# Performance work log

Hardware: AMD Instinct MI355X
Metric: run time of the kernel (lower is better)

Reference implementation:

```python
import jax, jax.numpy as jnp
import numpy as np

B, T, IN, CELL, OUT = 512, 32, 512, 128, 128


def setup_inputs() -> dict:
    key = jax.random.key(0)
    ks = jax.random.split(key, 6)
    d = IN + CELL
    w = lambda k, shape, fan: jax.random.normal(k, shape, jnp.float32) / np.sqrt(fan).astype(np.float32)
    return {
        "x": jax.random.normal(ks[0], (B, T, IN), jnp.float32),
        "Wf": w(ks[1], (d, CELL), d), "bf": jnp.zeros((CELL,), jnp.float32),
        "Wi1": w(ks[2], (d, CELL), d), "bi1": jnp.zeros((CELL,), jnp.float32),
        "Wi2": w(ks[3], (d, CELL), d), "bi2": jnp.zeros((CELL,), jnp.float32),
        "Wo": w(ks[4], (d, CELL), d), "bo": jnp.zeros((CELL,), jnp.float32),
        "Wc": w(ks[5], (CELL, OUT), CELL), "bc": jnp.zeros((OUT,), jnp.float32),
    }


def reference(x, Wf, bf, Wi1, bi1, Wi2, bi2, Wo, bo, Wc, bc):
    # Faithful to MyLSTM.forward: loop runs x.shape[1] times; each iteration
    # concatenates the FULL [B,T,CELL] cell_state with the FULL [B,T,IN] x
    # (x is never sliced per step). Only the last iteration's output matters,
    # but we carry it through the scan to match the loop structure exactly.
    Tn = x.shape[1]
    c0 = jnp.zeros(x.shape[:2] + (Wf.shape[1],), x.dtype)
    out0 = jnp.zeros(x.shape[:2] + (Wc.shape[1],), x.dtype)

    def step(carry, _):
        c, _prev_out = carry
        inp = jnp.concatenate([c, x], axis=-1)  # [B,T,CELL+IN]
        f = jax.nn.sigmoid(inp @ Wf + bf)
        c = c * f + jax.nn.sigmoid(inp @ Wi1 + bi1) * jnp.tanh(inp @ Wi2 + bi2)
        o = jax.nn.sigmoid(inp @ Wo + bo) * jnp.tanh(c)
        out = jax.nn.softmax(o @ Wc + bc, axis=2)  # out_features != 1 branch
        return (c, out), None

    (c, out), _ = jax.lax.scan(step, (c0, out0), None, length=Tn)
    return out, c
```

## Files before the change

### kernel.cpp

```cpp
#include <hip/hip_runtime.h>
#include <stdint.h>

#define ROWS  16384
#define CELL  128
#define INF   512
#define RPB   16
#define NSTEP 32

typedef _Float16 f16x8 __attribute__((ext_vector_type(8)));
typedef _Float16 f16x4 __attribute__((ext_vector_type(4)));
typedef float    f32x4 __attribute__((ext_vector_type(4)));

#define MFMA16(a, b, c) __builtin_amdgcn_mfma_f32_16x16x32_f16((a), (b), (c), 0, 0, 0)

#define AOFF  0
#define XOFF  65536
#define WCOFF 327680
#define WSTOT 344064

#define LOG2E  1.44269504f
#define LOG2E2 2.88539008f

__device__ __forceinline__ unsigned short f2h_bits(float f) {
  _Float16 h = (_Float16)f;
  return *(unsigned short*)&h;
}
__device__ __forceinline__ float sig2(float z) {
  return __builtin_amdgcn_rcpf(1.f + __builtin_amdgcn_exp2f(-z));
}
__device__ __forceinline__ float tanh2(float z) {
  return 1.f - 2.f * __builtin_amdgcn_rcpf(__builtin_amdgcn_exp2f(z) + 1.f);
}

__global__ __launch_bounds__(256) void prep_kernel(
    const float* __restrict__ Wf, const float* __restrict__ Wi1,
    const float* __restrict__ Wi2, const float* __restrict__ Wo,
    const float* __restrict__ Wc, unsigned short* __restrict__ ws) {
  int id = blockIdx.x * blockDim.x + threadIdx.x;
  if (id >= WSTOT) return;
  const float* Wg[4] = {Wf, Wi1, Wi2, Wo};
  const float scl[4] = {LOG2E, LOG2E, LOG2E2, LOG2E};
  float v;
  int k, n, base;
  if (id < XOFF) {
    int g = id >> 14, r = id & 16383;
    k = r >> 7; n = r & 127;
    v = Wg[g][k * CELL + n] * scl[g];
    base = g * 16384;
  } else if (id < WCOFF) {
    int t = id - XOFF;
    int g = t >> 16, r = t & 65535;
    k = r >> 7; n = r & 127;
    v = Wg[g][(CELL + k) * CELL + n] * scl[g];
    base = XOFF + g * 65536;
  } else {
    int r = id - WCOFF;
    k = r >> 7; n = r & 127;
    v = Wc[k * CELL + n];
    base = WCOFF;
  }
  int ks = k >> 5, kk = k & 31;
  int lane = ((kk >> 3) << 4) | (n & 15);
  int j = kk & 7, nb = n >> 4;
  ws[base + ((ks * 8 + nb) * 64 + lane) * 8 + j] = f2h_bits(v);
}

__global__ __launch_bounds__(512, 4) void lstm_kernel(
    const float* __restrict__ x,
    const float* __restrict__ bf_, const float* __restrict__ bi1,
    const float* __restrict__ bi2, const float* __restrict__ bo,
    const float* __restrict__ bc,
    const unsigned short* __restrict__ ws, float* __restrict__ out) {

  __shared__ _Float16 cF[2][16][136];
  __shared__ union {
    _Float16 xs[16][520];
    struct {
      float    s[16][132];
      _Float16 o[16][136];
    } ep;
  } uS;

  const int tid  = threadIdx.x;
  const int lane = tid & 63;
  const int w    = tid >> 6;
  const int n16  = lane & 15;
  const int g4   = lane >> 4;
  const int col0 = w * 16 + g4 * 4;
  const int r0   = blockIdx.x * RPB;

  const _Float16* Aw  = (const _Float16*)ws + AOFF;
  const _Float16* Xw  = (const _Float16*)ws + XOFF;
  const _Float16* Wcw = (const _Float16*)ws + WCOFF;

  {
    const float* xb = x + (size_t)r0 * INF;
#pragma unroll
    for (int i = 0; i < 4; ++i) {
      int flat = tid + i * 512;
      int row = flat >> 7, c4 = flat & 127;
      const float4 v = ((const float4*)(xb + (size_t)row * INF))[c4];
      f16x4 h = {(_Float16)v.x, (_Float16)v.y, (_Float16)v.z, (_Float16)v.w};
      *(f16x4*)&uS.xs[row][c4 * 4] = h;
    }
  }
  __syncthreads();

  f32x4 u[4];
#pragma unroll
  for (int g = 0; g < 4; ++g)
#pragma unroll
    for (int i = 0; i < 4; ++i) u[g][i] = 0.f;

#pragma unroll 4
  for (int ks = 0; ks < 16; ++ks) {
    f16x8 a = *(const f16x8*)&uS.xs[n16][ks * 32 + g4 * 8];
#pragma unroll
    for (int g = 0; g < 4; ++g) {
      f16x8 b = *(const f16x8*)(Xw + g * 65536 + ((ks * 8 + w) * 64 + lane) * 8);
      u[g] = MFMA16(b, a, u[g]);
    }
  }
  {
    f32x4 b0 = *(const f32x4*)&bf_[col0];
    f32x4 b1 = *(const f32x4*)&bi1[col0];
    f32x4 b2 = *(const f32x4*)&bi2[col0];
    f32x4 b3 = *(const f32x4*)&bo[col0];
#pragma unroll
    for (int i = 0; i < 4; ++i) {
      u[0][i] = fmaf(b0[i], LOG2E,  u[0][i]);
      u[1][i] = fmaf(b1[i], LOG2E,  u[1][i]);
      u[2][i] = fmaf(b2[i], LOG2E2, u[2][i]);
      u[3][i] = fmaf(b3[i], LOG2E,  u[3][i]);
    }
  }

  f16x8 wr[3][4];
#pragma unroll
  for (int g = 0; g < 3; ++g)
#pragma unroll
    for (int ks = 0; ks < 4; ++ks)
      wr[g][ks] = *(const f16x8*)(Aw + g * 16384 + ((ks * 8 + w) * 64 + lane) * 8);

  f32x4 cr;
  {
    f16x4 hv;
#pragma unroll
    for (int i = 0; i < 4; ++i) {
      float c0 = sig2(u[1][i]) * tanh2(u[2][i]);
      cr[i] = c0;
      hv[i] = (_Float16)c0;
    }
    *(f16x4*)&cF[0][n16][col0] = hv;
  }
  __syncthreads();

#pragma unroll 1
  for (int t = 1; t < NSTEP - 1; ++t) {
    const int rb = (t + 1) & 1, wb = t & 1;
    f16x8 a[4];
#pragma unroll
    for (int ks = 0; ks < 4; ++ks)
      a[ks] = *(const f16x8*)&cF[rb][n16][ks * 32 + g4 * 8];
    f32x4 zf = u[0], zi1 = u[1], zi2 = u[2];
#pragma unroll
    for (int ks = 0; ks < 4; ++ks) {
      zf  = MFMA16(wr[0][ks], a[ks], zf);
      zi1 = MFMA16(wr[1][ks], a[ks], zi1);
      zi2 = MFMA16(wr[2][ks], a[ks], zi2);
    }
    f16x4 hv;
#pragma unroll
    for (int i = 0; i < 4; ++i) {
      float fg = sig2(zf[i]);
      float ig = sig2(zi1[i]);
      float gg = tanh2(zi2[i]);
      float cn = fmaf(cr[i], fg, ig * gg);
      cr[i] = cn;
      hv[i] = (_Float16)cn;
    }
    *(f16x4*)&cF[wb][n16][col0] = hv;
    __syncthreads();
  }

  {
    f16x8 a[4];
#pragma unroll
    for (int ks = 0; ks < 4; ++ks)
      a[ks] = *(const f16x8*)&cF[0][n16][ks * 32 + g4 * 8];
    f32x4 zf = u[0], zi1 = u[1], zi2 = u[2], zo = u[3];
#pragma unroll
    for (int ks = 0; ks < 4; ++ks) {
      f16x8 bo_frag = *(const f16x8*)(Aw + 3 * 16384 + ((ks * 8 + w) * 64 + lane) * 8);
      zf  = MFMA16(wr[0][ks], a[ks], zf);
      zi1 = MFMA16(wr[1][ks], a[ks], zi1);
      zi2 = MFMA16(wr[2][ks], a[ks], zi2);
      zo  = MFMA16(bo_frag,  a[ks], zo);
    }
    f16x4 hv;
#pragma unroll
    for (int i = 0; i < 4; ++i) {
      float fg = sig2(zf[i]);
      float ig = sig2(zi1[i]);
      float gg = tanh2(zi2[i]);
      float cn = fmaf(cr[i], fg, ig * gg);
      cr[i] = cn;
      float ov = sig2(zo[i]) * tanh2(cn * LOG2E2);
      hv[i] = (_Float16)ov;
    }
    __syncthreads();
    *(f16x4*)&uS.ep.o[n16][col0] = hv;
    __syncthreads();
  }

  {
    f32x4 sacc;
#pragma unroll
    for (int i = 0; i < 4; ++i) sacc[i] = 0.f;
#pragma unroll
    for (int ks = 0; ks < 4; ++ks) {
      f16x8 a = *(const f16x8*)&uS.ep.o[n16][ks * 32 + g4 * 8];
      f16x8 b = *(const f16x8*)(Wcw + ((ks * 8 + w) * 64 + lane) * 8);
      sacc = MFMA16(b, a, sacc);
    }
    f32x4 bcv = *(const f32x4*)&bc[col0];
#pragma unroll
    for (int i = 0; i < 4; ++i) sacc[i] += bcv[i];
    *(f32x4*)&uS.ep.s[n16][col0] = sacc;
    __syncthreads();

#pragma unroll
    for (int rr = 0; rr < 2; ++rr) {
      int r = w * 2 + rr;
      float v0 = uS.ep.s[r][lane];
      float v1 = uS.ep.s[r][lane + 64];
      float m = fmaxf(v0, v1);
#pragma unroll
      for (int off = 32; off; off >>= 1) m = fmaxf(m, __shfl_xor(m, off, 64));
      float e0 = __expf(v0 - m), e1 = __expf(v1 - m);
      float sm = e0 + e1;
#pragma unroll
      for (int off = 32; off; off >>= 1) sm += __shfl_xor(sm, off, 64);
      float inv = __builtin_amdgcn_rcpf(sm);
      size_t base = (size_t)(r0 + r) * 128;
      out[base + lane]      = e0 * inv;
      out[base + lane + 64] = e1 * inv;
    }

    *(f32x4*)&out[(size_t)ROWS * 128 + (size_t)(r0 + n16) * 128 + col0] = cr;
  }
}

extern "C" void kernel_launch(void* const* d_in, const int* in_sizes, int n_in,
                              void* d_out, int out_size, void* d_ws, size_t ws_size,
                              hipStream_t stream) {
  const float* x   = (const float*)d_in[0];
  const float* Wf  = (const float*)d_in[1];
  const float* bf_ = (const float*)d_in[2];
  const float* Wi1 = (const float*)d_in[3];
  const float* bi1 = (const float*)d_in[4];
  const float* Wi2 = (const float*)d_in[5];
  const float* bi2 = (const float*)d_in[6];
  const float* Wo  = (const float*)d_in[7];
  const float* bo  = (const float*)d_in[8];
  const float* Wc  = (const float*)d_in[9];
  const float* bc  = (const float*)d_in[10];
  unsigned short* ws = (unsigned short*)d_ws;
  float* out = (float*)d_out;

  hipLaunchKernelGGL(prep_kernel, dim3((WSTOT + 255) / 256), dim3(256), 0, stream,
                     Wf, Wi1, Wi2, Wo, Wc, ws);
  hipLaunchKernelGGL(lstm_kernel, dim3(ROWS / RPB), dim3(512), 0, stream,
                     x, bf_, bi1, bi2, bo, bc, ws, out);
}
```

Measured before the change: 168.5 us.

## Split x staging around input GEMM, drop softmax max pass, raise MFMA priority

The x tile load is split in two halves so the second half's fp16 conversion and LDS store happen after the first half of the input-projection MFMAs, overlapping global load latency with compute. The softmax drops the max-reduction by folding log2e into Wc and applying exp2 directly to the logits, relying on the output being a bounded tanh·sigmoid value times small weights. The recurrent MFMA chains are written out explicitly, and s_setprio is raised around them. The final-step Wo fragments are now loaded all at once before the MFMAs. The softmax without max subtraction risks overflow for inputs where logits are large.

```diff
diff --git a/kernel.cpp b/kernel.cpp
--- a/kernel.cpp
+++ b/kernel.cpp
@@ -56,7 +56,7 @@
   } else {
     int r = id - WCOFF;
     k = r >> 7; n = r & 127;
-    v = Wc[k * CELL + n];
+    v = Wc[k * CELL + n] * LOG2E;
     base = WCOFF;
   }
   int ks = k >> 5, kk = k & 31;
@@ -76,7 +76,7 @@
   __shared__ union {
     _Float16 xs[16][520];
     struct {
-      float    s[16][132];
+      float    e[16][132];
       _Float16 o[16][136];
     } ep;
   } uS;
@@ -93,16 +93,21 @@
   const _Float16* Xw  = (const _Float16*)ws + XOFF;
   const _Float16* Wcw = (const _Float16*)ws + WCOFF;
 
-  {
-    const float* xb = x + (size_t)r0 * INF;
-#pragma unroll
-    for (int i = 0; i < 4; ++i) {
-      int flat = tid + i * 512;
-      int row = flat >> 7, c4 = flat & 127;
-      const float4 v = ((const float4*)(xb + (size_t)row * INF))[c4];
-      f16x4 h = {(_Float16)v.x, (_Float16)v.y, (_Float16)v.z, (_Float16)v.w};
-      *(f16x4*)&uS.xs[row][c4 * 4] = h;
-    }
+  const float* xb = x + (size_t)r0 * INF;
+  float4 v0a, v0b, v1a, v1b;
+  {
+    int fa = tid, fb = tid + 512;
+    int ra = fa >> 6, ca = fa & 63;
+    int rb_ = fb >> 6, cb = fb & 63;
+    const float4* pa = (const float4*)(xb + (size_t)ra * INF);
+    const float4* pb = (const float4*)(xb + (size_t)rb_ * INF);
+    v0a = pa[ca];       v0b = pb[cb];
+    v1a = pa[ca + 64];  v1b = pb[cb + 64];
+    f16x4 h;
+    h = (f16x4){(_Float16)v0a.x, (_Float16)v0a.y, (_Float16)v0a.z, (_Float16)v0a.w};
+    *(f16x4*)&uS.xs[ra][ca * 4] = h;
+    h = (f16x4){(_Float16)v0b.x, (_Float16)v0b.y, (_Float16)v0b.z, (_Float16)v0b.w};
+    *(f16x4*)&uS.xs[rb_][cb * 4] = h;
   }
   __syncthreads();
 
@@ -113,7 +118,29 @@
     for (int i = 0; i < 4; ++i) u[g][i] = 0.f;
 
 #pragma unroll 4
-  for (int ks = 0; ks < 16; ++ks) {
+  for (int ks = 0; ks < 8; ++ks) {
+    f16x8 a = *(const f16x8*)&uS.xs[n16][ks * 32 + g4 * 8];
+#pragma unroll
+    for (int g = 0; g < 4; ++g) {
+      f16x8 b = *(const f16x8*)(Xw + g * 65536 + ((ks * 8 + w) * 64 + lane) * 8);
+      u[g] = MFMA16(b, a, u[g]);
+    }
+  }
+
+  {
+    int fa = tid, fb = tid + 512;
+    int ra = fa >> 6, ca = fa & 63;
+    int rb_ = fb >> 6, cb = fb & 63;
+    f16x4 h;
+    h = (f16x4){(_Float16)v1a.x, (_Float16)v1a.y, (_Float16)v1a.z, (_Float16)v1a.w};
+    *(f16x4*)&uS.xs[ra][256 + ca * 4] = h;
+    h = (f16x4){(_Float16)v1b.x, (_Float16)v1b.y, (_Float16)v1b.z, (_Float16)v1b.w};
+    *(f16x4*)&uS.xs[rb_][256 + cb * 4] = h;
+  }
+  __syncthreads();
+
+#pragma unroll 4
+  for (int ks = 8; ks < 16; ++ks) {
     f16x8 a = *(const f16x8*)&uS.xs[n16][ks * 32 + g4 * 8];
 #pragma unroll
     for (int g = 0; g < 4; ++g) {
@@ -157,18 +184,25 @@
 
 #pragma unroll 1
   for (int t = 1; t < NSTEP - 1; ++t) {
-    const int rb = (t + 1) & 1, wb = t & 1;
-    f16x8 a[4];
-#pragma unroll
-    for (int ks = 0; ks < 4; ++ks)
-      a[ks] = *(const f16x8*)&cF[rb][n16][ks * 32 + g4 * 8];
-    f32x4 zf = u[0], zi1 = u[1], zi2 = u[2];
-#pragma unroll
-    for (int ks = 0; ks < 4; ++ks) {
-      zf  = MFMA16(wr[0][ks], a[ks], zf);
-      zi1 = MFMA16(wr[1][ks], a[ks], zi1);
-      zi2 = MFMA16(wr[2][ks], a[ks], zi2);
-    }
+    const _Float16* rd = &cF[(t + 1) & 1][n16][0];
+    f16x8 a0 = *(const f16x8*)(rd + g4 * 8);
+    f16x8 a1 = *(const f16x8*)(rd + 32 + g4 * 8);
+    f16x8 a2 = *(const f16x8*)(rd + 64 + g4 * 8);
+    f16x8 a3 = *(const f16x8*)(rd + 96 + g4 * 8);
+    __builtin_amdgcn_s_setprio(1);
+    f32x4 zf  = MFMA16(wr[0][0], a0, u[0]);
+    f32x4 zi1 = MFMA16(wr[1][0], a0, u[1]);
+    f32x4 zi2 = MFMA16(wr[2][0], a0, u[2]);
+    zf  = MFMA16(wr[0][1], a1, zf);
+    zi1 = MFMA16(wr[1][1], a1, zi1);
+    zi2 = MFMA16(wr[2][1], a1, zi2);
+    zf  = MFMA16(wr[0][2], a2, zf);
+    zi1 = MFMA16(wr[1][2], a2, zi1);
+    zi2 = MFMA16(wr[2][2], a2, zi2);
+    zf  = MFMA16(wr[0][3], a3, zf);
+    zi1 = MFMA16(wr[1][3], a3, zi1);
+    zi2 = MFMA16(wr[2][3], a3, zi2);
+    __builtin_amdgcn_s_setprio(0);
     f16x4 hv;
 #pragma unroll
     for (int i = 0; i < 4; ++i) {
@@ -179,24 +213,38 @@
       cr[i] = cn;
       hv[i] = (_Float16)cn;
     }
-    *(f16x4*)&cF[wb][n16][col0] = hv;
+    *(f16x4*)&cF[t & 1][n16][col0] = hv;
     __syncthreads();
   }
 
   {
-    f16x8 a[4];
-#pragma unroll
-    for (int ks = 0; ks < 4; ++ks)
-      a[ks] = *(const f16x8*)&cF[0][n16][ks * 32 + g4 * 8];
-    f32x4 zf = u[0], zi1 = u[1], zi2 = u[2], zo = u[3];
-#pragma unroll
-    for (int ks = 0; ks < 4; ++ks) {
-      f16x8 bo_frag = *(const f16x8*)(Aw + 3 * 16384 + ((ks * 8 + w) * 64 + lane) * 8);
-      zf  = MFMA16(wr[0][ks], a[ks], zf);
-      zi1 = MFMA16(wr[1][ks], a[ks], zi1);
-      zi2 = MFMA16(wr[2][ks], a[ks], zi2);
-      zo  = MFMA16(bo_frag,  a[ks], zo);
-    }
+    const _Float16* rd = &cF[0][n16][0];
+    f16x8 a0 = *(const f16x8*)(rd + g4 * 8);
+    f16x8 a1 = *(const f16x8*)(rd + 32 + g4 * 8);
+    f16x8 a2 = *(const f16x8*)(rd + 64 + g4 * 8);
+    f16x8 a3 = *(const f16x8*)(rd + 96 + g4 * 8);
+    f16x8 bo0 = *(const f16x8*)(Aw + 3 * 16384 + ((0 * 8 + w) * 64 + lane) * 8);
+    f16x8 bo1 = *(const f16x8*)(Aw + 3 * 16384 + ((1 * 8 + w) * 64 + lane) * 8);
+    f16x8 bo2 = *(const f16x8*)(Aw + 3 * 16384 + ((2 * 8 + w) * 64 + lane) * 8);
+    f16x8 bo3 = *(const f16x8*)(Aw + 3 * 16384 + ((3 * 8 + w) * 64 + lane) * 8);
+    __builtin_amdgcn_s_setprio(1);
+    f32x4 zf  = MFMA16(wr[0][0], a0, u[0]);
+    f32x4 zi1 = MFMA16(wr[1][0], a0, u[1]);
+    f32x4 zi2 = MFMA16(wr[2][0], a0, u[2]);
+    f32x4 zo  = MFMA16(bo0,      a0, u[3]);
+    zf  = MFMA16(wr[0][1], a1, zf);
+    zi1 = MFMA16(wr[1][1], a1, zi1);
+    zi2 = MFMA16(wr[2][1], a1, zi2);
+    zo  = MFMA16(bo1,      a1, zo);
+    zf  = MFMA16(wr[0][2], a2, zf);
+    zi1 = MFMA16(wr[1][2], a2, zi1);
+    zi2 = MFMA16(wr[2][2], a2, zi2);
+    zo  = MFMA16(bo2,      a2, zo);
+    zf  = MFMA16(wr[0][3], a3, zf);
+    zi1 = MFMA16(wr[1][3], a3, zi1);
+    zi2 = MFMA16(wr[2][3], a3, zi2);
+    zo  = MFMA16(bo3,      a3, zo);
+    __builtin_amdgcn_s_setprio(0);
     f16x4 hv;
 #pragma unroll
     for (int i = 0; i < 4; ++i) {
@@ -224,20 +272,18 @@
       sacc = MFMA16(b, a, sacc);
     }
     f32x4 bcv = *(const f32x4*)&bc[col0];
-#pragma unroll
-    for (int i = 0; i < 4; ++i) sacc[i] += bcv[i];
-    *(f32x4*)&uS.ep.s[n16][col0] = sacc;
+    f32x4 ev;
+#pragma unroll
+    for (int i = 0; i < 4; ++i)
+      ev[i] = __builtin_amdgcn_exp2f(fmaf(bcv[i], LOG2E, sacc[i]));
+    *(f32x4*)&uS.ep.e[n16][col0] = ev;
     __syncthreads();
 
 #pragma unroll
     for (int rr = 0; rr < 2; ++rr) {
       int r = w * 2 + rr;
-      float v0 = uS.ep.s[r][lane];
-      float v1 = uS.ep.s[r][lane + 64];
-      float m = fmaxf(v0, v1);
-#pragma unroll
-      for (int off = 32; off; off >>= 1) m = fmaxf(m, __shfl_xor(m, off, 64));
-      float e0 = __expf(v0 - m), e1 = __expf(v1 - m);
+      float e0 = uS.ep.e[r][lane];
+      float e1 = uS.ep.e[r][lane + 64];
       float sm = e0 + e1;
 #pragma unroll
       for (int off = 32; off; off >>= 1) sm += __shfl_xor(sm, off, 64);
```

Result: slower. 174.0 us (+3.3%).
